# Kernel optimization log

Hardware: AMD Instinct MI355X
Metric: run time of the kernel (lower is better)

## Reference

```python
import jax, jax.numpy as jnp
import numpy as np

B, T, C = 4, 1024, 2048
H, HKV, HD = 32, 8, 64
HID = 5632  # round_up(8*2048/3, 256)
EPS = 1e-6


def rmsnorm(x, scale):
    return x * scale * jax.lax.rsqrt(jnp.mean(x * x, axis=-1, keepdims=True) + EPS)


def rotary(t, cos, sin):
    # interleaved even/odd rotation, matching torch apply_rotary_emb
    te, to = t[..., ::2], t[..., 1::2]
    return jnp.stack((te * cos - to * sin, te * sin + to * cos), axis=-1).reshape(t.shape)


def setup_inputs() -> dict:
    key = jax.random.key(0)
    ks = jax.random.split(key, 8)
    s = 0.02
    inv = 1.0 / (10000.0 ** (np.arange(0, HD, 2, dtype=np.float64) / HD))
    ang = np.arange(T, dtype=np.float64)[:, None] * inv[None, :]
    return {
        "x": jax.random.normal(ks[0], (B, T, C), jnp.float32),
        "cos": jnp.asarray(np.cos(ang), jnp.float32),
        "sin": jnp.asarray(np.sin(ang), jnp.float32),
        "w_attn": jax.random.normal(ks[1], (C, (H + 2 * HKV) * HD), jnp.float32) * s,
        "w_proj": jax.random.normal(ks[2], (C, C), jnp.float32) * s,
        "w_gate": jax.random.normal(ks[3], (C, HID), jnp.float32) * s,
        "w_up": jax.random.normal(ks[4], (C, HID), jnp.float32) * s,
        "w_down": jax.random.normal(ks[5], (HID, C), jnp.float32) * s,
        "scale1": jnp.ones((C,), jnp.float32),
        "scale2": jnp.ones((C,), jnp.float32),
    }


def reference(x, cos, sin, w_attn, w_proj, w_gate, w_up, w_down, scale1, scale2):
    n_rep = H // HKV
    # --- attention block ---
    h = rmsnorm(x, scale1)
    qkv = h @ w_attn  # [B,T,(H+2*HKV)*HD]
    q, k, v = jnp.split(qkv, [H * HD, (H + HKV) * HD], axis=-1)
    q = q.reshape(B, T, H, HD).transpose(0, 2, 1, 3)      # [B,H,T,HD]
    k = k.reshape(B, T, HKV, HD).transpose(0, 2, 1, 3)    # [B,HKV,T,HD]
    v = v.reshape(B, T, HKV, HD).transpose(0, 2, 1, 3)
    q = rotary(q, cos, sin)
    k = rotary(k, cos, sin)
    # GQA: group q heads over kv heads instead of repeat_interleave
    qg = q.reshape(B, HKV, n_rep, T, HD)
    scores = jnp.einsum('bgrtd,bgsd->bgrts', qg, k) / jnp.sqrt(jnp.float32(HD))
    causal = jnp.tril(jnp.ones((T, T), bool))
    scores = jnp.where(causal, scores, jnp.finfo(scores.dtype).min)
    p = jax.nn.softmax(scores, axis=-1)
    y = jnp.einsum('bgrts,bgsd->bgrtd', p, v)
    y = y.reshape(B, H, T, HD).transpose(0, 2, 1, 3).reshape(B, T, C)
    x = x + y @ w_proj
    # --- SwiGLU MLP block ---
    h2 = rmsnorm(x, scale2)
    x = x + (jax.nn.silu(h2 @ w_gate) * (h2 @ w_up)) @ w_down
    return x
```

## Files before the change

kernel.cpp:

```cpp
#include <hip/hip_runtime.h>
#include <stdint.h>

#define B_ 4
#define T_ 1024
#define C_ 2048
#define H_ 32
#define HKV_ 8
#define HD_ 64
#define HID_ 5632

typedef __attribute__((ext_vector_type(8))) short short8;
typedef __attribute__((ext_vector_type(4))) float floatx4;

__device__ __forceinline__ float b2f(short s) {
  unsigned u = ((unsigned)(unsigned short)s) << 16;
  return __uint_as_float(u);
}
__device__ __forceinline__ short f2b(float f) {
  unsigned u = __float_as_uint(f);
  u = u + 0x7fffu + ((u >> 16) & 1u);
  return (short)(u >> 16);
}

#define GL2LDS(gp, lp)                                              \
  __builtin_amdgcn_global_load_lds(                                 \
      (const __attribute__((address_space(1))) void*)(gp),          \
      (__attribute__((address_space(3))) void*)(lp), 16, 0, 0)

__global__ __launch_bounds__(256) void convt_kernel(
    const float* __restrict__ W, short* __restrict__ Wt, int K, int N) {
  __shared__ short t[32][33];
  int n0 = blockIdx.x * 32, k0 = blockIdx.y * 32;
  int tx = threadIdx.x & 31, ty = threadIdx.x >> 5;
#pragma unroll
  for (int j = 0; j < 4; ++j)
    t[ty + j * 8][tx] = f2b(W[(size_t)(k0 + ty + j * 8) * N + n0 + tx]);
  __syncthreads();
#pragma unroll
  for (int j = 0; j < 4; ++j)
    Wt[(size_t)(n0 + ty + j * 8) * K + k0 + tx] = t[tx][ty + j * 8];
}

__global__ __launch_bounds__(256) void vt_kernel(
    const short* __restrict__ vin, short* __restrict__ vout) {
  __shared__ short t[32][33];
  int t0 = blockIdx.x * 32, d0 = blockIdx.y * 32, bg = blockIdx.z;
  int tx = threadIdx.x & 31, ty = threadIdx.x >> 5;
  const short* src = vin + (size_t)bg * T_ * HD_;
  short* dst = vout + (size_t)bg * T_ * HD_;
#pragma unroll
  for (int j = 0; j < 4; ++j)
    t[ty + j * 8][tx] = src[(size_t)(t0 + ty + j * 8) * HD_ + d0 + tx];
  __syncthreads();
#pragma unroll
  for (int j = 0; j < 4; ++j)
    dst[(size_t)(d0 + ty + j * 8) * T_ + t0 + tx] = t[tx][ty + j * 8];
}

__global__ __launch_bounds__(256) void rmsnorm_kernel(
    const float* __restrict__ x, const float* __restrict__ scale,
    short* __restrict__ out) {
  int row = blockIdx.x, tid = threadIdx.x;
  const float4* xr = (const float4*)(x + (size_t)row * C_);
  float4 v0 = xr[tid], v1 = xr[tid + 256];
  float s = v0.x * v0.x + v0.y * v0.y + v0.z * v0.z + v0.w * v0.w +
            v1.x * v1.x + v1.y * v1.y + v1.z * v1.z + v1.w * v1.w;
  for (int off = 32; off > 0; off >>= 1) s += __shfl_down(s, off, 64);
  __shared__ float red[4];
  if ((tid & 63) == 0) red[tid >> 6] = s;
  __syncthreads();
  float tot = red[0] + red[1] + red[2] + red[3];
  float r = rsqrtf(tot * (1.0f / (float)C_) + 1e-6f);
  const float4* sc = (const float4*)scale;
  float4 s0 = sc[tid], s1 = sc[tid + 256];
  short* o = out + (size_t)row * C_;
  o[tid * 4 + 0] = f2b(v0.x * s0.x * r);
  o[tid * 4 + 1] = f2b(v0.y * s0.y * r);
  o[tid * 4 + 2] = f2b(v0.z * s0.z * r);
  o[tid * 4 + 3] = f2b(v0.w * s0.w * r);
  o[1024 + tid * 4 + 0] = f2b(v1.x * s1.x * r);
  o[1024 + tid * 4 + 1] = f2b(v1.y * s1.y * r);
  o[1024 + tid * 4 + 2] = f2b(v1.z * s1.z * r);
  o[1024 + tid * 4 + 3] = f2b(v1.w * s1.w * r);
}

template <int EPI>
__global__ __launch_bounds__(256, 2) void gemm128_kernel(
    const short* __restrict__ A, const short* __restrict__ Bt,
    void* __restrict__ Out, const float* __restrict__ resid,
    int M, int N, int K) {
  __shared__ __align__(16) short smem[16384];
  short* As = smem;
  short* Bs = smem + 8192;
  int tid = threadIdx.x, lane = tid & 63, wave = tid >> 6;
  int quad = lane >> 4, l16 = lane & 15;
  int m0 = blockIdx.y * 128, n0 = blockIdx.x * 128;
  int wm = (wave & 1) * 64, wn = (wave >> 1) * 64;

  const short* ap[4];
  const short* bp[4];
  short* lA[4];
  short* lB[4];
#pragma unroll
  for (int c = 0; c < 4; ++c) {
    int S = wave * 256 + c * 64 + lane;
    int row = S >> 3, kc = ((S & 7) - (row & 7)) & 7;
    ap[c] = A + (size_t)(m0 + row) * K + kc * 8;
    bp[c] = Bt + (size_t)(n0 + row) * K + kc * 8;
    lA[c] = As + (wave * 256 + c * 64) * 8;
    lB[c] = Bs + (wave * 256 + c * 64) * 8;
  }

  int aoff[4], boff[4];
#pragma unroll
  for (int i = 0; i < 4; ++i) {
    int ra = wm + i * 16 + l16;
    aoff[i] = (ra * 8 + ((quad + ra) & 7)) * 8;
    int rb = wn + i * 16 + l16;
    boff[i] = (rb * 8 + ((quad + rb) & 7)) * 8;
  }

  floatx4 acc[4][4] = {};
  for (int k0 = 0; k0 < K; k0 += 64) {
#pragma unroll
    for (int c = 0; c < 4; ++c) {
      GL2LDS(ap[c] + k0, lA[c]);
      GL2LDS(bp[c] + k0, lB[c]);
    }
    __syncthreads();
#pragma unroll
    for (int h = 0; h < 2; ++h) {
      short8 af[4], bf[4];
#pragma unroll
      for (int i = 0; i < 4; ++i) af[i] = *(const short8*)(As + (aoff[i] ^ (h * 32)));
#pragma unroll
      for (int i = 0; i < 4; ++i) bf[i] = *(const short8*)(Bs + (boff[i] ^ (h * 32)));
#pragma unroll
      for (int mi = 0; mi < 4; ++mi)
#pragma unroll
        for (int ni = 0; ni < 4; ++ni)
          acc[mi][ni] = __builtin_amdgcn_mfma_f32_16x16x32_bf16(
              af[mi], bf[ni], acc[mi][ni], 0, 0, 0);
    }
    __syncthreads();
  }
#pragma unroll
  for (int mi = 0; mi < 4; ++mi)
#pragma unroll
    for (int ni = 0; ni < 4; ++ni)
#pragma unroll
      for (int r = 0; r < 4; ++r) {
        int row = m0 + wm + mi * 16 + quad * 4 + r;
        int col = n0 + wn + ni * 16 + l16;
        size_t idx = (size_t)row * N + col;
        float a = acc[mi][ni][r];
        if constexpr (EPI == 0)
          ((short*)Out)[idx] = f2b(a);
        else
          ((float*)Out)[idx] = resid[idx] + a;
      }
}

__global__ __launch_bounds__(256, 2) void gateup_kernel(
    const short* __restrict__ A, const short* __restrict__ Wg,
    const short* __restrict__ Wu, short* __restrict__ act, int K) {
  __shared__ __align__(16) short smem[16384];
  short* As = smem;
  short* Bs = smem + 8192;
  int tid = threadIdx.x, lane = tid & 63, wave = tid >> 6;
  int quad = lane >> 4, l16 = lane & 15;
  int m0 = blockIdx.y * 128, n0 = blockIdx.x * 64;
  int wm = (wave & 1) * 64, half = wave >> 1;
  int half_stage = wave >> 1;

  const short* ap[4];
  const short* bp[4];
  short* lA[4];
  short* lB[4];
  const short* Bsel = half_stage ? Wu : Wg;
#pragma unroll
  for (int c = 0; c < 4; ++c) {
    int S = wave * 256 + c * 64 + lane;
    int row = S >> 3, kc = ((S & 7) - (row & 7)) & 7;
    ap[c] = A + (size_t)(m0 + row) * K + kc * 8;
    bp[c] = Bsel + (size_t)(n0 + row - half_stage * 64) * K + kc * 8;
    lA[c] = As + (wave * 256 + c * 64) * 8;
    lB[c] = Bs + (wave * 256 + c * 64) * 8;
  }

  int aoff[4], boff[4];
#pragma unroll
  for (int i = 0; i < 4; ++i) {
    int ra = wm + i * 16 + l16;
    aoff[i] = (ra * 8 + ((quad + ra) & 7)) * 8;
    int rb = half * 64 + i * 16 + l16;
    boff[i] = (rb * 8 + ((quad + rb) & 7)) * 8;
  }

  floatx4 acc[4][4] = {};
  for (int k0 = 0; k0 < K; k0 += 64) {
#pragma unroll
    for (int c = 0; c < 4; ++c) {
      GL2LDS(ap[c] + k0, lA[c]);
      GL2LDS(bp[c] + k0, lB[c]);
    }
    __syncthreads();
#pragma unroll
    for (int h = 0; h < 2; ++h) {
      short8 af[4], bf[4];
#pragma unroll
      for (int i = 0; i < 4; ++i) af[i] = *(const short8*)(As + (aoff[i] ^ (h * 32)));
#pragma unroll
      for (int i = 0; i < 4; ++i) bf[i] = *(const short8*)(Bs + (boff[i] ^ (h * 32)));
#pragma unroll
      for (int mi = 0; mi < 4; ++mi)
#pragma unroll
        for (int ni = 0; ni < 4; ++ni)
          acc[mi][ni] = __builtin_amdgcn_mfma_f32_16x16x32_bf16(
              af[mi], bf[ni], acc[mi][ni], 0, 0, 0);
    }
    __syncthreads();
  }
  short* Ex = smem;
  if (half == 1) {
#pragma unroll
    for (int mi = 0; mi < 4; ++mi)
#pragma unroll
      for (int ni = 0; ni < 4; ++ni)
#pragma unroll
        for (int r = 0; r < 4; ++r)
          Ex[(wm + mi * 16 + quad * 4 + r) * 64 + ni * 16 + l16] =
              f2b(acc[mi][ni][r]);
  }
  __syncthreads();
  if (half == 0) {
#pragma unroll
    for (int mi = 0; mi < 4; ++mi)
#pragma unroll
      for (int ni = 0; ni < 4; ++ni)
#pragma unroll
        for (int r = 0; r < 4; ++r) {
          int row = wm + mi * 16 + quad * 4 + r;
          int col = ni * 16 + l16;
          float u = b2f(Ex[row * 64 + col]);
          float g = acc[mi][ni][r];
          float a = g / (1.0f + __expf(-g)) * u;
          act[(size_t)(m0 + row) * HID_ + n0 + col] = f2b(a);
        }
  }
}

__global__ __launch_bounds__(256) void rope_kernel(
    const short* __restrict__ qkv, const float* __restrict__ cosp,
    const float* __restrict__ sinp, short* __restrict__ q,
    short* __restrict__ k, short* __restrict__ v) {
  int idx = blockIdx.x * 256 + threadIdx.x;
  int i = idx & 31;
  int rest = idx >> 5;
  int head = rest % 48;
  int rest2 = rest / 48;
  int t = rest2 & 1023;
  int b = rest2 >> 10;
  const short* src = qkv + (size_t)(b * T_ + t) * 3072 + head * 64 + 2 * i;
  float e = b2f(src[0]), o = b2f(src[1]);
  if (head < 32) {
    float c = cosp[t * 32 + i], s = sinp[t * 32 + i];
    short* dst = q + ((size_t)(b * 32 + head) * 1024 + t) * 64 + 2 * i;
    dst[0] = f2b((e * c - o * s) * 0.125f);
    dst[1] = f2b((e * s + o * c) * 0.125f);
  } else if (head < 40) {
    float c = cosp[t * 32 + i], s = sinp[t * 32 + i];
    short* dst = k + ((size_t)(b * 8 + (head - 32)) * 1024 + t) * 64 + 2 * i;
    dst[0] = f2b(e * c - o * s);
    dst[1] = f2b(e * s + o * c);
  } else {
    short* dst = v + ((size_t)(b * 8 + (head - 40)) * 1024 + t) * 64 + 2 * i;
    dst[0] = src[0];
    dst[1] = src[1];
  }
}

__global__ __launch_bounds__(256) void attn_kernel(
    const short* __restrict__ q, const short* __restrict__ k,
    const short* __restrict__ vt, short* __restrict__ y) {
  __shared__ __align__(16) short P[4][640];
  int bx = blockIdx.x, h = blockIdx.y, b = blockIdx.z;
  int lane = threadIdx.x & 63, wave = threadIdx.x >> 6;
  int quad = lane >> 4, l16 = lane & 15;
  int g = h >> 2;
  const short* qp = q + (size_t)(b * H_ + h) * T_ * HD_;
  const short* kp = k + (size_t)(b * HKV_ + g) * T_ * HD_;
  const short* vp = vt + (size_t)(b * HKV_ + g) * T_ * HD_;
  int q0 = bx * 64 + wave * 16;
  short8 qf0 = *(const short8*)(qp + (q0 + l16) * HD_ + quad * 8);
  short8 qf1 = *(const short8*)(qp + (q0 + l16) * HD_ + 32 + quad * 8);
  floatx4 acc[4] = {};
  float m_r[4] = {-1e30f, -1e30f, -1e30f, -1e30f};
  float l_r[4] = {0.f, 0.f, 0.f, 0.f};
  int qi[4];
#pragma unroll
  for (int r = 0; r < 4; ++r) qi[r] = q0 + quad * 4 + r;
  for (int k0 = 0; k0 < q0 + 16; k0 += 32) {
    floatx4 s0 = {0.f, 0.f, 0.f, 0.f}, s1 = {0.f, 0.f, 0.f, 0.f};
    short8 kf0 = *(const short8*)(kp + (k0 + l16) * HD_ + quad * 8);
    short8 kf0b = *(const short8*)(kp + (k0 + l16) * HD_ + 32 + quad * 8);
    s0 = __builtin_amdgcn_mfma_f32_16x16x32_bf16(qf0, kf0, s0, 0, 0, 0);
    s0 = __builtin_amdgcn_mfma_f32_16x16x32_bf16(qf1, kf0b, s0, 0, 0, 0);
    short8 kf1 = *(const short8*)(kp + (k0 + 16 + l16) * HD_ + quad * 8);
    short8 kf1b = *(const short8*)(kp + (k0 + 16 + l16) * HD_ + 32 + quad * 8);
    s1 = __builtin_amdgcn_mfma_f32_16x16x32_bf16(qf0, kf1, s1, 0, 0, 0);
    s1 = __builtin_amdgcn_mfma_f32_16x16x32_bf16(qf1, kf1b, s1, 0, 0, 0);
    float p0[4], p1[4], mt[4];
#pragma unroll
    for (int r = 0; r < 4; ++r) {
      p0[r] = (k0 + l16 <= qi[r]) ? s0[r] : -1e30f;
      p1[r] = (k0 + 16 + l16 <= qi[r]) ? s1[r] : -1e30f;
      mt[r] = fmaxf(p0[r], p1[r]);
    }
#pragma unroll
    for (int off = 1; off < 16; off <<= 1) {
#pragma unroll
      for (int r = 0; r < 4; ++r) mt[r] = fmaxf(mt[r], __shfl_xor(mt[r], off, 64));
    }
    float alpha[4];
#pragma unroll
    for (int r = 0; r < 4; ++r) {
      float mn = fmaxf(m_r[r], mt[r]);
      alpha[r] = __expf(m_r[r] - mn);
      m_r[r] = mn;
      p0[r] = __expf(p0[r] - mn);
      p1[r] = __expf(p1[r] - mn);
    }
    float rs[4];
#pragma unroll
    for (int r = 0; r < 4; ++r) rs[r] = p0[r] + p1[r];
#pragma unroll
    for (int off = 1; off < 16; off <<= 1) {
#pragma unroll
      for (int r = 0; r < 4; ++r) rs[r] += __shfl_xor(rs[r], off, 64);
    }
#pragma unroll
    for (int r = 0; r < 4; ++r) l_r[r] = l_r[r] * alpha[r] + rs[r];
#pragma unroll
    for (int n = 0; n < 4; ++n)
#pragma unroll
      for (int r = 0; r < 4; ++r) acc[n][r] *= alpha[r];
#pragma unroll
    for (int r = 0; r < 4; ++r) {
      P[wave][(quad * 4 + r) * 40 + l16] = f2b(p0[r]);
      P[wave][(quad * 4 + r) * 40 + 16 + l16] = f2b(p1[r]);
    }
    short8 pf = *(const short8*)(&P[wave][l16 * 40 + quad * 8]);
#pragma unroll
    for (int n = 0; n < 4; ++n) {
      short8 vf = *(const short8*)(vp + (size_t)(n * 16 + l16) * T_ + k0 + quad * 8);
      acc[n] = __builtin_amdgcn_mfma_f32_16x16x32_bf16(pf, vf, acc[n], 0, 0, 0);
    }
  }
#pragma unroll
  for (int n = 0; n < 4; ++n)
#pragma unroll
    for (int r = 0; r < 4; ++r) {
      int t = q0 + quad * 4 + r;
      y[(size_t)(b * T_ + t) * C_ + h * 64 + n * 16 + l16] = f2b(acc[n][r] / l_r[r]);
    }
}

extern "C" void kernel_launch(void* const* d_in, const int* in_sizes, int n_in,
                              void* d_out, int out_size, void* d_ws, size_t ws_size,
                              hipStream_t stream) {
  const float* x = (const float*)d_in[0];
  const float* cosp = (const float*)d_in[1];
  const float* sinp = (const float*)d_in[2];
  const float* w_attn = (const float*)d_in[3];
  const float* w_proj = (const float*)d_in[4];
  const float* w_gate = (const float*)d_in[5];
  const float* w_up = (const float*)d_in[6];
  const float* w_down = (const float*)d_in[7];
  const float* scale1 = (const float*)d_in[8];
  const float* scale2 = (const float*)d_in[9];
  float* out = (float*)d_out;
  char* ws = (char*)d_ws;

  short* S1 = (short*)(ws + 0);
  short* S2 = (short*)(ws + 23068672);
  short* hbuf = (short*)(ws + 46137344);
  short* S0 = (short*)(ws + 62914560);
  short* qkv = (short*)(ws + 75497472);
  short* kbuf = (short*)(ws + 100663296);
  short* vbuf = (short*)(ws + 104857600);
  short* vtbuf = (short*)(ws + 109051904);
  short* act = (short*)(ws + 62914560);

  convt_kernel<<<dim3(3072 / 32, 2048 / 32), 256, 0, stream>>>(w_attn, S0, 2048, 3072);
  rmsnorm_kernel<<<4096, 256, 0, stream>>>(x, scale1, hbuf);
  gemm128_kernel<0><<<dim3(3072 / 128, 4096 / 128), 256, 0, stream>>>(
      hbuf, S0, qkv, nullptr, 4096, 3072, 2048);
  rope_kernel<<<24576, 256, 0, stream>>>(qkv, cosp, sinp, hbuf, kbuf, vbuf);
  vt_kernel<<<dim3(32, 2, 32), 256, 0, stream>>>(vbuf, vtbuf);
  attn_kernel<<<dim3(16, 32, 4), 256, 0, stream>>>(hbuf, kbuf, vtbuf, qkv);
  convt_kernel<<<dim3(2048 / 32, 2048 / 32), 256, 0, stream>>>(w_proj, S0, 2048, 2048);
  gemm128_kernel<1><<<dim3(2048 / 128, 4096 / 128), 256, 0, stream>>>(
      qkv, S0, out, x, 4096, 2048, 2048);
  rmsnorm_kernel<<<4096, 256, 0, stream>>>(out, scale2, hbuf);
  convt_kernel<<<dim3(5632 / 32, 2048 / 32), 256, 0, stream>>>(w_gate, S1, 2048, 5632);
  convt_kernel<<<dim3(5632 / 32, 2048 / 32), 256, 0, stream>>>(w_up, S2, 2048, 5632);
  gateup_kernel<<<dim3(5632 / 64, 4096 / 128), 256, 0, stream>>>(hbuf, S1, S2, act, 2048);
  convt_kernel<<<dim3(2048 / 32, 5632 / 32), 256, 0, stream>>>(w_down, S1, 5632, 2048);
  gemm128_kernel<1><<<dim3(2048 / 128, 4096 / 128), 256, 0, stream>>>(
      act, S1, out, out, 4096, 2048, 5632);
}
```

Baseline: 889.9 us.

## Rework attention to 64-key tiles with causal load balancing and widen transpose stores

The attention kernel now processes 64 keys per step and computes the transposed S^T = K·Q^T, so each lane holds one query column and the row reductions need only two cross-lane shuffles. Each block handles a query tile and its mirror (15-bx) to even out causal work, which halves the grid. P goes through a swizzled LDS tile with packed stores, and output is written via LDS as 16-byte vectors. The weight conversion/transpose kernel now uses 64x64 tiles with packed bf16 pairs and uint4 stores, reducing store transactions at the cost of more LDS and registers.

```diff
diff --git a/kernel.cpp b/kernel.cpp
--- a/kernel.cpp
+++ b/kernel.cpp
@@ -21,6 +21,10 @@
   u = u + 0x7fffu + ((u >> 16) & 1u);
   return (short)(u >> 16);
 }
+__device__ __forceinline__ unsigned pk2(float a, float b) {
+  return ((unsigned)(unsigned short)f2b(a)) |
+         ((unsigned)(unsigned short)f2b(b) << 16);
+}
 
 #define GL2LDS(gp, lp)                                              \
   __builtin_amdgcn_global_load_lds(                                 \
@@ -29,16 +33,24 @@
 
 __global__ __launch_bounds__(256) void convt_kernel(
     const float* __restrict__ W, short* __restrict__ Wt, int K, int N) {
-  __shared__ short t[32][33];
-  int n0 = blockIdx.x * 32, k0 = blockIdx.y * 32;
-  int tx = threadIdx.x & 31, ty = threadIdx.x >> 5;
-#pragma unroll
-  for (int j = 0; j < 4; ++j)
-    t[ty + j * 8][tx] = f2b(W[(size_t)(k0 + ty + j * 8) * N + n0 + tx]);
+  __shared__ unsigned u[32][65];
+  int n0 = blockIdx.x * 64, k0 = blockIdx.y * 64;
+  int tx = threadIdx.x & 63, ty = threadIdx.x >> 6;
+#pragma unroll
+  for (int j = 0; j < 8; ++j) {
+    int kpair = ty * 8 + j;
+    float lo = W[(size_t)(k0 + 2 * kpair) * N + n0 + tx];
+    float hi = W[(size_t)(k0 + 2 * kpair + 1) * N + n0 + tx];
+    u[kpair][tx] = pk2(lo, hi);
+  }
   __syncthreads();
-#pragma unroll
-  for (int j = 0; j < 4; ++j)
-    Wt[(size_t)(n0 + ty + j * 8) * K + k0 + tx] = t[tx][ty + j * 8];
+  int ny = threadIdx.x >> 2, kx = threadIdx.x & 3;
+  unsigned vals[8];
+#pragma unroll
+  for (int i = 0; i < 8; ++i) vals[i] = u[kx * 8 + i][ny];
+  uint4* dst = (uint4*)(Wt + (size_t)(n0 + ny) * K + k0 + kx * 16);
+  dst[0] = make_uint4(vals[0], vals[1], vals[2], vals[3]);
+  dst[1] = make_uint4(vals[4], vals[5], vals[6], vals[7]);
 }
 
 __global__ __launch_bounds__(256) void vt_kernel(
@@ -283,7 +295,7 @@
 __global__ __launch_bounds__(256) void attn_kernel(
     const short* __restrict__ q, const short* __restrict__ k,
     const short* __restrict__ vt, short* __restrict__ y) {
-  __shared__ __align__(16) short P[4][640];
+  __shared__ __align__(16) short P[4][1024];
   int bx = blockIdx.x, h = blockIdx.y, b = blockIdx.z;
   int lane = threadIdx.x & 63, wave = threadIdx.x >> 6;
   int quad = lane >> 4, l16 = lane & 15;
@@ -291,79 +303,98 @@
   const short* qp = q + (size_t)(b * H_ + h) * T_ * HD_;
   const short* kp = k + (size_t)(b * HKV_ + g) * T_ * HD_;
   const short* vp = vt + (size_t)(b * HKV_ + g) * T_ * HD_;
-  int q0 = bx * 64 + wave * 16;
-  short8 qf0 = *(const short8*)(qp + (q0 + l16) * HD_ + quad * 8);
-  short8 qf1 = *(const short8*)(qp + (q0 + l16) * HD_ + 32 + quad * 8);
-  floatx4 acc[4] = {};
-  float m_r[4] = {-1e30f, -1e30f, -1e30f, -1e30f};
-  float l_r[4] = {0.f, 0.f, 0.f, 0.f};
-  int qi[4];
-#pragma unroll
-  for (int r = 0; r < 4; ++r) qi[r] = q0 + quad * 4 + r;
-  for (int k0 = 0; k0 < q0 + 16; k0 += 32) {
-    floatx4 s0 = {0.f, 0.f, 0.f, 0.f}, s1 = {0.f, 0.f, 0.f, 0.f};
-    short8 kf0 = *(const short8*)(kp + (k0 + l16) * HD_ + quad * 8);
-    short8 kf0b = *(const short8*)(kp + (k0 + l16) * HD_ + 32 + quad * 8);
-    s0 = __builtin_amdgcn_mfma_f32_16x16x32_bf16(qf0, kf0, s0, 0, 0, 0);
-    s0 = __builtin_amdgcn_mfma_f32_16x16x32_bf16(qf1, kf0b, s0, 0, 0, 0);
-    short8 kf1 = *(const short8*)(kp + (k0 + 16 + l16) * HD_ + quad * 8);
-    short8 kf1b = *(const short8*)(kp + (k0 + 16 + l16) * HD_ + 32 + quad * 8);
-    s1 = __builtin_amdgcn_mfma_f32_16x16x32_bf16(qf0, kf1, s1, 0, 0, 0);
-    s1 = __builtin_amdgcn_mfma_f32_16x16x32_bf16(qf1, kf1b, s1, 0, 0, 0);
-    float p0[4], p1[4], mt[4];
-#pragma unroll
-    for (int r = 0; r < 4; ++r) {
-      p0[r] = (k0 + l16 <= qi[r]) ? s0[r] : -1e30f;
-      p1[r] = (k0 + 16 + l16 <= qi[r]) ? s1[r] : -1e30f;
-      mt[r] = fmaxf(p0[r], p1[r]);
-    }
-#pragma unroll
-    for (int off = 1; off < 16; off <<= 1) {
-#pragma unroll
-      for (int r = 0; r < 4; ++r) mt[r] = fmaxf(mt[r], __shfl_xor(mt[r], off, 64));
-    }
-    float alpha[4];
-#pragma unroll
-    for (int r = 0; r < 4; ++r) {
-      float mn = fmaxf(m_r[r], mt[r]);
-      alpha[r] = __expf(m_r[r] - mn);
-      m_r[r] = mn;
-      p0[r] = __expf(p0[r] - mn);
-      p1[r] = __expf(p1[r] - mn);
-    }
-    float rs[4];
-#pragma unroll
-    for (int r = 0; r < 4; ++r) rs[r] = p0[r] + p1[r];
-#pragma unroll
-    for (int off = 1; off < 16; off <<= 1) {
-#pragma unroll
-      for (int r = 0; r < 4; ++r) rs[r] += __shfl_xor(rs[r], off, 64);
-    }
-#pragma unroll
-    for (int r = 0; r < 4; ++r) l_r[r] = l_r[r] * alpha[r] + rs[r];
-#pragma unroll
-    for (int n = 0; n < 4; ++n)
-#pragma unroll
-      for (int r = 0; r < 4; ++r) acc[n][r] *= alpha[r];
-#pragma unroll
-    for (int r = 0; r < 4; ++r) {
-      P[wave][(quad * 4 + r) * 40 + l16] = f2b(p0[r]);
-      P[wave][(quad * 4 + r) * 40 + 16 + l16] = f2b(p1[r]);
-    }
-    short8 pf = *(const short8*)(&P[wave][l16 * 40 + quad * 8]);
-#pragma unroll
-    for (int n = 0; n < 4; ++n) {
-      short8 vf = *(const short8*)(vp + (size_t)(n * 16 + l16) * T_ + k0 + quad * 8);
-      acc[n] = __builtin_amdgcn_mfma_f32_16x16x32_bf16(pf, vf, acc[n], 0, 0, 0);
-    }
-  }
-#pragma unroll
-  for (int n = 0; n < 4; ++n)
-#pragma unroll
-    for (int r = 0; r < 4; ++r) {
-      int t = q0 + quad * 4 + r;
-      y[(size_t)(b * T_ + t) * C_ + h * 64 + n * 16 + l16] = f2b(acc[n][r] / l_r[r]);
-    }
+  short* Pw = &P[wave][0];
+  int sw = (l16 & 7) << 1;
+#pragma unroll 1
+  for (int half = 0; half < 2; ++half) {
+    int tb = half ? (15 - bx) : bx;
+    int q0w = tb * 64 + wave * 16;
+    int qidx = q0w + l16;
+    short8 qf0 = *(const short8*)(qp + (size_t)(q0w + l16) * HD_ + quad * 8);
+    short8 qf1 = *(const short8*)(qp + (size_t)(q0w + l16) * HD_ + 32 + quad * 8);
+    floatx4 acc[4] = {};
+    float m = -1e30f, l = 0.f;
+    for (int k0 = 0; k0 <= q0w; k0 += 64) {
+      floatx4 st[4];
+#pragma unroll
+      for (int kt = 0; kt < 4; ++kt) {
+        floatx4 z = {0.f, 0.f, 0.f, 0.f};
+        const short* kb = kp + (size_t)(k0 + kt * 16 + l16) * HD_;
+        short8 kf0 = *(const short8*)(kb + quad * 8);
+        short8 kf1 = *(const short8*)(kb + 32 + quad * 8);
+        z = __builtin_amdgcn_mfma_f32_16x16x32_bf16(kf0, qf0, z, 0, 0, 0);
+        z = __builtin_amdgcn_mfma_f32_16x16x32_bf16(kf1, qf1, z, 0, 0, 0);
+        st[kt] = z;
+      }
+      if (k0 + 64 > q0w) {
+#pragma unroll
+        for (int kt = 0; kt < 4; ++kt)
+#pragma unroll
+          for (int r = 0; r < 4; ++r)
+            if (k0 + kt * 16 + quad * 4 + r > qidx) st[kt][r] = -1e30f;
+      }
+      float mloc = -1e30f;
+#pragma unroll
+      for (int kt = 0; kt < 4; ++kt)
+#pragma unroll
+        for (int r = 0; r < 4; ++r) mloc = fmaxf(mloc, st[kt][r]);
+      mloc = fmaxf(mloc, __shfl_xor(mloc, 16, 64));
+      mloc = fmaxf(mloc, __shfl_xor(mloc, 32, 64));
+      float mn = fmaxf(m, mloc);
+      float alpha = __expf(m - mn);
+      m = mn;
+      float rsum = 0.f;
+#pragma unroll
+      for (int kt = 0; kt < 4; ++kt)
+#pragma unroll
+        for (int r = 0; r < 4; ++r) {
+          float p = __expf(st[kt][r] - mn);
+          st[kt][r] = p;
+          rsum += p;
+        }
+      rsum += __shfl_xor(rsum, 16, 64);
+      rsum += __shfl_xor(rsum, 32, 64);
+      l = l * alpha + rsum;
+#pragma unroll
+      for (int mt = 0; mt < 4; ++mt)
+#pragma unroll
+        for (int r = 0; r < 4; ++r) acc[mt][r] *= alpha;
+#pragma unroll
+      for (int kt = 0; kt < 4; ++kt) {
+        int hc = (kt * 4 + quad) ^ sw;
+        *(uint2*)(Pw + l16 * 64 + hc * 4) =
+            make_uint2(pk2(st[kt][0], st[kt][1]), pk2(st[kt][2], st[kt][3]));
+      }
+#pragma unroll
+      for (int chunk = 0; chunk < 2; ++chunk) {
+        int hc = (chunk * 8 + quad * 2) ^ sw;
+        short8 pf = *(const short8*)(Pw + l16 * 64 + hc * 4);
+#pragma unroll
+        for (int mt = 0; mt < 4; ++mt) {
+          short8 vf = *(const short8*)(vp + (size_t)(mt * 16 + l16) * T_ +
+                                       k0 + chunk * 32 + quad * 8);
+          acc[mt] =
+              __builtin_amdgcn_mfma_f32_16x16x32_bf16(vf, pf, acc[mt], 0, 0, 0);
+        }
+      }
+    }
+    float inv = 1.0f / l;
+#pragma unroll
+    for (int mt = 0; mt < 4; ++mt) {
+      int hc = (mt * 4 + quad) ^ sw;
+      *(uint2*)(Pw + l16 * 64 + hc * 4) =
+          make_uint2(pk2(acc[mt][0] * inv, acc[mt][1] * inv),
+                     pk2(acc[mt][2] * inv, acc[mt][3] * inv));
+    }
+    uint2 o0 = *(uint2*)(Pw + l16 * 64 + (((quad * 4 + 0) ^ sw) * 4));
+    uint2 o1 = *(uint2*)(Pw + l16 * 64 + (((quad * 4 + 1) ^ sw) * 4));
+    uint2 o2 = *(uint2*)(Pw + l16 * 64 + (((quad * 4 + 2) ^ sw) * 4));
+    uint2 o3 = *(uint2*)(Pw + l16 * 64 + (((quad * 4 + 3) ^ sw) * 4));
+    uint4* dst =
+        (uint4*)(y + (size_t)(b * T_ + q0w + l16) * C_ + h * 64 + quad * 16);
+    dst[0] = make_uint4(o0.x, o0.y, o1.x, o1.y);
+    dst[1] = make_uint4(o2.x, o2.y, o3.x, o3.y);
+  }
 }
 
 extern "C" void kernel_launch(void* const* d_in, const int* in_sizes, int n_in,
@@ -392,21 +423,21 @@
   short* vtbuf = (short*)(ws + 109051904);
   short* act = (short*)(ws + 62914560);
 
-  convt_kernel<<<dim3(3072 / 32, 2048 / 32), 256, 0, stream>>>(w_attn, S0, 2048, 3072);
+  convt_kernel<<<dim3(3072 / 64, 2048 / 64), 256, 0, stream>>>(w_attn, S0, 2048, 3072);
   rmsnorm_kernel<<<4096, 256, 0, stream>>>(x, scale1, hbuf);
   gemm128_kernel<0><<<dim3(3072 / 128, 4096 / 128), 256, 0, stream>>>(
       hbuf, S0, qkv, nullptr, 4096, 3072, 2048);
   rope_kernel<<<24576, 256, 0, stream>>>(qkv, cosp, sinp, hbuf, kbuf, vbuf);
   vt_kernel<<<dim3(32, 2, 32), 256, 0, stream>>>(vbuf, vtbuf);
-  attn_kernel<<<dim3(16, 32, 4), 256, 0, stream>>>(hbuf, kbuf, vtbuf, qkv);
-  convt_kernel<<<dim3(2048 / 32, 2048 / 32), 256, 0, stream>>>(w_proj, S0, 2048, 2048);
+  attn_kernel<<<dim3(8, 32, 4), 256, 0, stream>>>(hbuf, kbuf, vtbuf, qkv);
+  convt_kernel<<<dim3(2048 / 64, 2048 / 64), 256, 0, stream>>>(w_proj, S0, 2048, 2048);
   gemm128_kernel<1><<<dim3(2048 / 128, 4096 / 128), 256, 0, stream>>>(
       qkv, S0, out, x, 4096, 2048, 2048);
   rmsnorm_kernel<<<4096, 256, 0, stream>>>(out, scale2, hbuf);
-  convt_kernel<<<dim3(5632 / 32, 2048 / 32), 256, 0, stream>>>(w_gate, S1, 2048, 5632);
-  convt_kernel<<<dim3(5632 / 32, 2048 / 32), 256, 0, stream>>>(w_up, S2, 2048, 5632);
+  convt_kernel<<<dim3(5632 / 64, 2048 / 64), 256, 0, stream>>>(w_gate, S1, 2048, 5632);
+  convt_kernel<<<dim3(5632 / 64, 2048 / 64), 256, 0, stream>>>(w_up, S2, 2048, 5632);
   gateup_kernel<<<dim3(5632 / 64, 4096 / 128), 256, 0, stream>>>(hbuf, S1, S2, act, 2048);
-  convt_kernel<<<dim3(2048 / 32, 5632 / 32), 256, 0, stream>>>(w_down, S1, 5632, 2048);
+  convt_kernel<<<dim3(2048 / 64, 5632 / 64), 256, 0, stream>>>(w_down, S1, 5632, 2048);
   gemm128_kernel<1><<<dim3(2048 / 128, 4096 / 128), 256, 0, stream>>>(
       act, S1, out, out, 4096, 2048, 5632);
 }
```

Result: faster. 789.4 us (-11.3%).
